# Kernel optimization log

Measured on AMD Instinct MI355X. Metric: run time of the kernel, lower is better.

The kernel has to match this reference:

```python
import jax, jax.numpy as jnp
import numpy as np


def setup_inputs() -> dict:
    key = jax.random.key(0)
    k1, k2, k3 = jax.random.split(key, 3)
    B, S, E = 2, 2048, 2048
    H, O, A = 16, 1024, 128  # heads, codebook options, head_size (E = H*A)
    x = jax.random.normal(k1, (B, S, E), dtype=jnp.float32)
    vq_head_weights = jax.random.normal(k2, (H, O, A), dtype=jnp.float32) * 0.02
    vq_codebooks = jax.random.normal(k3, (H, O, A), dtype=jnp.float32) * 0.02
    temperature = jnp.ones((1,), dtype=jnp.float32)
    return {"x": x, "vq_head_weights": vq_head_weights, "vq_codebooks": vq_codebooks, "temperature": temperature}


def reference(x, vq_head_weights, vq_codebooks, temperature):
    # Training-mode, frozen, use_temperature=True path (straight-through VQ):
    # probs = one_hot(argmax(logits)) + softmax(logits/T) - stop_grad(softmax(logits/T))
    B, S, E = x.shape
    H, O, A = vq_head_weights.shape
    x_prepped = x.reshape(B, S, H, A)
    logits = jnp.einsum('bsha,hoa->bsho', x_prepped, vq_head_weights)
    probs = jax.nn.softmax(logits / temperature[0], axis=-1)
    argmax = jnp.argmax(logits, axis=-1)  # [B,S,H]
    hard_probs = jax.nn.one_hot(argmax, O, dtype=logits.dtype)
    probs = hard_probs + probs - jax.lax.stop_gradient(probs)
    out = jnp.einsum('bsho,hoa->bsha', probs, vq_codebooks)
    return out.reshape(B, S, E)
```

## Files before the change

### kernel.cpp

```cpp
#include <hip/hip_runtime.h>

typedef _Float16 half8 __attribute__((ext_vector_type(8)));
typedef float    f32x16 __attribute__((ext_vector_type(16)));

constexpr int kH = 16;
constexpr int kO = 1024;
constexpr int kA = 128;
constexpr int kBS = 4096;
constexpr int MTILE = 64;
constexpr int NITER = 16;

__global__ void split_w(const float* __restrict__ w, ushort* __restrict__ wp) {
    const int lane = threadIdx.x & 63;
    const int gw   = blockIdx.x * 4 + (threadIdx.x >> 6);
    const int ks   = lane >> 3;
    const int half = (lane >> 2) & 1;
    const int j    = (2 * lane) & 7;
#pragma unroll
    for (int q = 0; q < 4; ++q) {
        int r = gw * 4 + q;
        int h = r >> 10, o = r & 1023, t = o >> 5, o31 = o & 31;
        float2 v = *(const float2*)(w + r * kA + lane * 2);
        _Float16 h0 = (_Float16)v.x, h1 = (_Float16)v.y;
        _Float16 l0 = (_Float16)(v.x - (float)h0), l1 = (_Float16)(v.y - (float)h1);
        ushort2 hv = { __builtin_bit_cast(ushort, h0), __builtin_bit_cast(ushort, h1) };
        ushort2 lv = { __builtin_bit_cast(ushort, l0), __builtin_bit_cast(ushort, l1) };
        ushort* d = wp + (h * 32 + t) * 8192 + ks * 512 + (half * 32 + o31) * 8 + j;
        *(ushort2*)d = hv;
        *(ushort2*)(d + 4096) = lv;
    }
}

__launch_bounds__(256, 4)
__global__ void vq_argmax_gather(const float* __restrict__ x,
                                 const ushort* __restrict__ wp,
                                 const float* __restrict__ cb,
                                 float* __restrict__ out) {
    __shared__ ushort xl_lds[4][8][512];
    __shared__ float red_max[2][MTILE];
    __shared__ int   red_idx[2][MTILE];

    const int tid   = threadIdx.x;
    const int lane  = tid & 63;
    const int wv    = tid >> 6;
    const int nhalf = wv >> 1;
    const int msub  = wv & 1;
    const int bid   = blockIdx.x;
    const int h  = ((bid & 7) << 1) | ((bid >> 3) & 1);
    const int p0 = (bid >> 4) * MTILE;

    const int l31  = lane & 31;
    const int half = lane >> 5;

    const ushort* wb = wp + (h * 32 + nhalf * 16) * 8192 + lane * 8;

    half8 A[8];
#pragma unroll
    for (int ks = 0; ks < 8; ++ks)
        A[ks] = *(const half8*)(wb + ks * 512);

    const int mrow = p0 + msub * 32 + l31;
    const float* xb = x + (mrow * kH + h) * kA + half * 8;
    half8 xh[8];
#pragma unroll
    for (int ks = 0; ks < 8; ++ks) {
        float4 v0 = *(const float4*)(xb + ks * 16);
        float4 v1 = *(const float4*)(xb + ks * 16 + 4);
        float va[8] = { v0.x, v0.y, v0.z, v0.w, v1.x, v1.y, v1.z, v1.w };
        half8 hi, lo;
#pragma unroll
        for (int j = 0; j < 8; ++j) {
            _Float16 hj = (_Float16)va[j];
            hi[j] = hj;
            lo[j] = (_Float16)(va[j] - (float)hj);
        }
        xh[ks] = hi;
        *(half8*)&xl_lds[wv][ks][lane * 8] = lo;
    }

    float best = -1e30f;
    int   bidx = 0;
    const int nwb = nhalf * (kO / 2);

    for (int it = 0; it < NITER; ++it) {
        const ushort* tb = wb + it * 8192;
        f32x16 acc = {};
#pragma unroll
        for (int ks = 0; ks < 8; ++ks)
            acc = __builtin_amdgcn_mfma_f32_32x32x16_f16(A[ks], xh[ks], acc, 0, 0, 0);
#pragma unroll
        for (int ks = 0; ks < 8; ++ks) {
            half8 xlk = *(const half8*)&xl_lds[wv][ks][lane * 8];
            acc = __builtin_amdgcn_mfma_f32_32x32x16_f16(A[ks], xlk, acc, 0, 0, 0);
        }
        half8 Bf[8];
#pragma unroll
        for (int ks = 0; ks < 8; ++ks)
            Bf[ks] = *(const half8*)(tb + 4096 + ks * 512);
#pragma unroll
        for (int ks = 0; ks < 8; ++ks)
            acc = __builtin_amdgcn_mfma_f32_32x32x16_f16(Bf[ks], xh[ks], acc, 0, 0, 0);
        if (it + 1 < NITER) {
            const ushort* nb = wb + (it + 1) * 8192;
#pragma unroll
            for (int ks = 0; ks < 8; ++ks)
                A[ks] = *(const half8*)(nb + ks * 512);
        }

        float lv = acc[0];
        int   lr = 0;
#pragma unroll
        for (int r = 1; r < 16; ++r)
            if (acc[r] > lv) { lv = acc[r]; lr = r; }
        int li = nwb + it * 32 + 4 * half + (lr & 3) + 8 * (lr >> 2);
        if (lv > best) { best = lv; bidx = li; }
    }

    {
        float om = __shfl_xor(best, 32, 64);
        int   oi = __shfl_xor(bidx, 32, 64);
        if (om > best || (om == best && oi < bidx)) { best = om; bidx = oi; }
    }
    if (half == 0) {
        red_max[nhalf][msub * 32 + l31] = best;
        red_idx[nhalf][msub * 32 + l31] = bidx;
    }
    __syncthreads();

    for (int i = tid; i < MTILE * 32; i += 256) {
        int row = i >> 5, ch = i & 31;
        float m0 = red_max[0][row], m1 = red_max[1][row];
        int o = (m1 > m0) ? red_idx[1][row] : red_idx[0][row];
        float4 v = *(const float4*)(cb + (h * kO + o) * kA + ch * 4);
        *(float4*)(out + ((p0 + row) * kH + h) * kA + ch * 4) = v;
    }
}

extern "C" void kernel_launch(void* const* d_in, const int* in_sizes, int n_in,
                              void* d_out, int out_size, void* d_ws, size_t ws_size,
                              hipStream_t stream) {
    const float* x  = (const float*)d_in[0];
    const float* w  = (const float*)d_in[1];
    const float* cb = (const float*)d_in[2];
    float* out = (float*)d_out;

    ushort* wpacked = (ushort*)d_ws;

    split_w<<<dim3(1024), dim3(256), 0, stream>>>(w, wpacked);
    vq_argmax_gather<<<dim3((kBS / MTILE) * kH), dim3(256), 0, stream>>>(x, wpacked, cb, out);
}
```

Before: 153.5 us.

## Keep weight tiles in registers and stream x chunks, combine argmax via atomics

Drops the separate weight pre-split kernel. Each wave now keeps a 64-option slice of W, split into fp16 hi/lo halves, resident in registers. The block then streams 512 positions of x through a double-buffered LDS tile and converts them to hi/lo on the fly. Partial argmax results across option chunks are merged with 64-bit atomicMax on packed (value, inverted index) keys, and a separate gather kernel reads the codebook rows. This cuts the weight-streaming bandwidth of the old kernel, at the cost of a memset, an extra launch, atomics, a barrier per x tile and lower occupancy (launch bounds of 2).

```diff
diff --git a/kernel.cpp b/kernel.cpp
--- a/kernel.cpp
+++ b/kernel.cpp
@@ -7,132 +7,160 @@
 constexpr int kO = 1024;
 constexpr int kA = 128;
 constexpr int kBS = 4096;
-constexpr int MTILE = 64;
-constexpr int NITER = 16;
+constexpr int PCHUNK = 512;
+constexpr int XT = PCHUNK / 32;
+constexpr int OPW = 64;
+constexpr int OCHUNK = 4 * OPW;
 
-__global__ void split_w(const float* __restrict__ w, ushort* __restrict__ wp) {
-    const int lane = threadIdx.x & 63;
-    const int gw   = blockIdx.x * 4 + (threadIdx.x >> 6);
-    const int ks   = lane >> 3;
-    const int half = (lane >> 2) & 1;
-    const int j    = (2 * lane) & 7;
+__device__ __forceinline__ void cvt44(float4 v0, float4 v1, half8& hi, half8& lo) {
+    float va[8] = { v0.x, v0.y, v0.z, v0.w, v1.x, v1.y, v1.z, v1.w };
 #pragma unroll
-    for (int q = 0; q < 4; ++q) {
-        int r = gw * 4 + q;
-        int h = r >> 10, o = r & 1023, t = o >> 5, o31 = o & 31;
-        float2 v = *(const float2*)(w + r * kA + lane * 2);
-        _Float16 h0 = (_Float16)v.x, h1 = (_Float16)v.y;
-        _Float16 l0 = (_Float16)(v.x - (float)h0), l1 = (_Float16)(v.y - (float)h1);
-        ushort2 hv = { __builtin_bit_cast(ushort, h0), __builtin_bit_cast(ushort, h1) };
-        ushort2 lv = { __builtin_bit_cast(ushort, l0), __builtin_bit_cast(ushort, l1) };
-        ushort* d = wp + (h * 32 + t) * 8192 + ks * 512 + (half * 32 + o31) * 8 + j;
-        *(ushort2*)d = hv;
-        *(ushort2*)(d + 4096) = lv;
+    for (int j = 0; j < 8; ++j) {
+        _Float16 hj = (_Float16)va[j];
+        hi[j] = hj;
+        lo[j] = (_Float16)(va[j] - (float)hj);
     }
 }
 
-__launch_bounds__(256, 4)
-__global__ void vq_argmax_gather(const float* __restrict__ x,
-                                 const ushort* __restrict__ wp,
-                                 const float* __restrict__ cb,
-                                 float* __restrict__ out) {
-    __shared__ ushort xl_lds[4][8][512];
-    __shared__ float red_max[2][MTILE];
-    __shared__ int   red_idx[2][MTILE];
+__launch_bounds__(256, 2)
+__global__ void vq_score(const float* __restrict__ x,
+                         const float* __restrict__ w,
+                         unsigned long long* __restrict__ keys) {
+    __shared__ ushort xfrag[2][2][8][512];
 
-    const int tid   = threadIdx.x;
-    const int lane  = tid & 63;
-    const int wv    = tid >> 6;
-    const int nhalf = wv >> 1;
-    const int msub  = wv & 1;
-    const int bid   = blockIdx.x;
-    const int h  = ((bid & 7) << 1) | ((bid >> 3) & 1);
-    const int p0 = (bid >> 4) * MTILE;
+    const int tid  = threadIdx.x;
+    const int lane = tid & 63;
+    const int wv   = tid >> 6;
+    const int bid  = blockIdx.x;
+    const int xcd = bid & 7;
+    const int r   = bid >> 3;
+    const int h   = (xcd << 1) | (r & 1);
+    const int oc  = (r >> 1) & 3;
+    const int pc  = r >> 3;
+    const int p0  = pc * PCHUNK;
+    const int obase = oc * OCHUNK + wv * OPW;
 
     const int l31  = lane & 31;
     const int half = lane >> 5;
 
-    const ushort* wb = wp + (h * 32 + nhalf * 16) * 8192 + lane * 8;
-
-    half8 A[8];
-#pragma unroll
-    for (int ks = 0; ks < 8; ++ks)
-        A[ks] = *(const half8*)(wb + ks * 512);
-
-    const int mrow = p0 + msub * 32 + l31;
-    const float* xb = x + (mrow * kH + h) * kA + half * 8;
-    half8 xh[8];
+    const float* wb = w + (h * kO + obase + l31) * kA + half * 8;
+    half8 wh0[8], wl0[8], wh1[8], wl1[8];
 #pragma unroll
     for (int ks = 0; ks < 8; ++ks) {
-        float4 v0 = *(const float4*)(xb + ks * 16);
-        float4 v1 = *(const float4*)(xb + ks * 16 + 4);
-        float va[8] = { v0.x, v0.y, v0.z, v0.w, v1.x, v1.y, v1.z, v1.w };
-        half8 hi, lo;
-#pragma unroll
-        for (int j = 0; j < 8; ++j) {
-            _Float16 hj = (_Float16)va[j];
-            hi[j] = hj;
-            lo[j] = (_Float16)(va[j] - (float)hj);
-        }
-        xh[ks] = hi;
-        *(half8*)&xl_lds[wv][ks][lane * 8] = lo;
+        float4 a0 = *(const float4*)(wb + ks * 16);
+        float4 a1 = *(const float4*)(wb + ks * 16 + 4);
+        cvt44(a0, a1, wh0[ks], wl0[ks]);
+        float4 b0 = *(const float4*)(wb + 32 * kA + ks * 16);
+        float4 b1 = *(const float4*)(wb + 32 * kA + ks * 16 + 4);
+        cvt44(b0, b1, wh1[ks], wl1[ks]);
     }
 
-    float best = -1e30f;
-    int   bidx = 0;
-    const int nwb = nhalf * (kO / 2);
-
-    for (int it = 0; it < NITER; ++it) {
-        const ushort* tb = wb + it * 8192;
-        f32x16 acc = {};
-#pragma unroll
-        for (int ks = 0; ks < 8; ++ks)
-            acc = __builtin_amdgcn_mfma_f32_32x32x16_f16(A[ks], xh[ks], acc, 0, 0, 0);
-#pragma unroll
-        for (int ks = 0; ks < 8; ++ks) {
-            half8 xlk = *(const half8*)&xl_lds[wv][ks][lane * 8];
-            acc = __builtin_amdgcn_mfma_f32_32x32x16_f16(A[ks], xlk, acc, 0, 0, 0);
-        }
-        half8 Bf[8];
-#pragma unroll
-        for (int ks = 0; ks < 8; ++ks)
-            Bf[ks] = *(const half8*)(tb + 4096 + ks * 512);
-#pragma unroll
-        for (int ks = 0; ks < 8; ++ks)
-            acc = __builtin_amdgcn_mfma_f32_32x32x16_f16(Bf[ks], xh[ks], acc, 0, 0, 0);
-        if (it + 1 < NITER) {
-            const ushort* nb = wb + (it + 1) * 8192;
-#pragma unroll
-            for (int ks = 0; ks < 8; ++ks)
-                A[ks] = *(const half8*)(nb + ks * 512);
-        }
-
-        float lv = acc[0];
-        int   lr = 0;
-#pragma unroll
-        for (int r = 1; r < 16; ++r)
-            if (acc[r] > lv) { lv = acc[r]; lr = r; }
-        int li = nwb + it * 32 + 4 * half + (lr & 3) + 8 * (lr >> 2);
-        if (lv > best) { best = lv; bidx = li; }
-    }
+    const int ls  = tid & 63;
+    const int ks0 = tid >> 6;
+    const float* xsrc = x + ((p0 + (ls & 31)) * kH + h) * kA + ks0 * 16 + (ls >> 5) * 8;
+    const int xtile_stride = 32 * kH * kA;
 
     {
-        float om = __shfl_xor(best, 32, 64);
-        int   oi = __shfl_xor(bidx, 32, 64);
-        if (om > best || (om == best && oi < bidx)) { best = om; bidx = oi; }
-    }
-    if (half == 0) {
-        red_max[nhalf][msub * 32 + l31] = best;
-        red_idx[nhalf][msub * 32 + l31] = bidx;
+        float4 n0a = *(const float4*)(xsrc);
+        float4 n0b = *(const float4*)(xsrc + 4);
+        float4 n1a = *(const float4*)(xsrc + 64);
+        float4 n1b = *(const float4*)(xsrc + 68);
+        half8 hi, lo;
+        cvt44(n0a, n0b, hi, lo);
+        *(half8*)&xfrag[0][0][ks0][ls * 8] = hi;
+        *(half8*)&xfrag[0][1][ks0][ls * 8] = lo;
+        cvt44(n1a, n1b, hi, lo);
+        *(half8*)&xfrag[0][0][ks0 + 4][ls * 8] = hi;
+        *(half8*)&xfrag[0][1][ks0 + 4][ls * 8] = lo;
     }
     __syncthreads();
 
-    for (int i = tid; i < MTILE * 32; i += 256) {
+    for (int xt = 0; xt < XT; ++xt) {
+        const int cur = xt & 1;
+
+        float4 n0a, n0b, n1a, n1b;
+        if (xt + 1 < XT) {
+            const float* np = xsrc + (xt + 1) * xtile_stride;
+            n0a = *(const float4*)(np);
+            n0b = *(const float4*)(np + 4);
+            n1a = *(const float4*)(np + 64);
+            n1b = *(const float4*)(np + 68);
+        }
+
+        f32x16 acc0 = {}, acc1 = {};
+#pragma unroll
+        for (int ks = 0; ks < 8; ++ks) {
+            half8 xh = *(const half8*)&xfrag[cur][0][ks][lane * 8];
+            acc0 = __builtin_amdgcn_mfma_f32_32x32x16_f16(wh0[ks], xh, acc0, 0, 0, 0);
+            acc1 = __builtin_amdgcn_mfma_f32_32x32x16_f16(wh1[ks], xh, acc1, 0, 0, 0);
+        }
+#pragma unroll
+        for (int ks = 0; ks < 8; ++ks) {
+            half8 xl = *(const half8*)&xfrag[cur][1][ks][lane * 8];
+            acc0 = __builtin_amdgcn_mfma_f32_32x32x16_f16(wh0[ks], xl, acc0, 0, 0, 0);
+            acc1 = __builtin_amdgcn_mfma_f32_32x32x16_f16(wh1[ks], xl, acc1, 0, 0, 0);
+        }
+#pragma unroll
+        for (int ks = 0; ks < 8; ++ks) {
+            half8 xh = *(const half8*)&xfrag[cur][0][ks][lane * 8];
+            acc0 = __builtin_amdgcn_mfma_f32_32x32x16_f16(wl0[ks], xh, acc0, 0, 0, 0);
+            acc1 = __builtin_amdgcn_mfma_f32_32x32x16_f16(wl1[ks], xh, acc1, 0, 0, 0);
+        }
+
+        if (xt + 1 < XT) {
+            const int nb = cur ^ 1;
+            half8 hi, lo;
+            cvt44(n0a, n0b, hi, lo);
+            *(half8*)&xfrag[nb][0][ks0][ls * 8] = hi;
+            *(half8*)&xfrag[nb][1][ks0][ls * 8] = lo;
+            cvt44(n1a, n1b, hi, lo);
+            *(half8*)&xfrag[nb][0][ks0 + 4][ls * 8] = hi;
+            *(half8*)&xfrag[nb][1][ks0 + 4][ls * 8] = lo;
+        }
+
+        float lv0 = acc0[0]; int lr0 = 0;
+#pragma unroll
+        for (int rr = 1; rr < 16; ++rr)
+            if (acc0[rr] > lv0) { lv0 = acc0[rr]; lr0 = rr; }
+        float lv1 = acc1[0]; int lr1 = 0;
+#pragma unroll
+        for (int rr = 1; rr < 16; ++rr)
+            if (acc1[rr] > lv1) { lv1 = acc1[rr]; lr1 = rr; }
+
+        float bv = lv0;
+        int   bo = obase + ((lr0 & 3) + 8 * (lr0 >> 2) + 4 * half);
+        int   o1 = obase + 32 + ((lr1 & 3) + 8 * (lr1 >> 2) + 4 * half);
+        if (lv1 > bv) { bv = lv1; bo = o1; }
+
+        float om = __shfl_xor(bv, 32, 64);
+        int   oi = __shfl_xor(bo, 32, 64);
+        if (om > bv || (om == bv && oi < bo)) { bv = om; bo = oi; }
+
+        if (half == 0) {
+            uint32_t vb   = __builtin_bit_cast(uint32_t, bv);
+            uint32_t mono = (vb & 0x80000000u) ? ~vb : (vb | 0x80000000u);
+            unsigned long long key =
+                ((unsigned long long)mono << 32) | (uint32_t)~(uint32_t)bo;
+            atomicMax(&keys[(p0 + xt * 32 + l31) * kH + h], key);
+        }
+
+        __syncthreads();
+    }
+}
+
+__launch_bounds__(256)
+__global__ void vq_gather(const unsigned long long* __restrict__ keys,
+                          const float* __restrict__ cb,
+                          float* __restrict__ out) {
+    const int total = kBS * kH * 32;
+    for (int i = blockIdx.x * blockDim.x + threadIdx.x; i < total;
+         i += gridDim.x * blockDim.x) {
         int row = i >> 5, ch = i & 31;
-        float m0 = red_max[0][row], m1 = red_max[1][row];
-        int o = (m1 > m0) ? red_idx[1][row] : red_idx[0][row];
-        float4 v = *(const float4*)(cb + (h * kO + o) * kA + ch * 4);
-        *(float4*)(out + ((p0 + row) * kH + h) * kA + ch * 4) = v;
+        unsigned long long k = keys[row];
+        int o = (int)(~(uint32_t)k) & (kO - 1);
+        int hh = row & (kH - 1);
+        float4 v = *(const float4*)(cb + (hh * kO + o) * kA + ch * 4);
+        *(float4*)(out + row * kA + ch * 4) = v;
     }
 }
 
@@ -144,8 +172,9 @@
     const float* cb = (const float*)d_in[2];
     float* out = (float*)d_out;
 
-    ushort* wpacked = (ushort*)d_ws;
+    unsigned long long* keys = (unsigned long long*)d_ws;
 
-    split_w<<<dim3(1024), dim3(256), 0, stream>>>(w, wpacked);
-    vq_argmax_gather<<<dim3((kBS / MTILE) * kH), dim3(256), 0, stream>>>(x, wpacked, cb, out);
+    hipMemsetAsync(keys, 0, (size_t)kBS * kH * 8, stream);
+    vq_score<<<dim3(512),  dim3(256), 0, stream>>>(x, w, keys);
+    vq_gather<<<dim3(2048), dim3(256), 0, stream>>>(keys, cb, out);
 }
```

After: 184.3 us. +20.1%, slower.
